# Kernel tuning notes

Hardware: AMD Instinct MI355X
Metric: run time of the kernel (lower is better)

Reference implementation:

```python
import jax, jax.numpy as jnp
import numpy as np

B, S, H, I, L, NH = 1, 256, 384, 1536, 2, 8

def _gelu(x):
    return jax.nn.gelu(x, approximate=False)  # torch nn.GELU default = exact erf

def _ln(x, g, b, eps=1e-5):
    m = x.mean(-1, keepdims=True)
    v = jnp.var(x, axis=-1, keepdims=True)
    return (x - m) / jnp.sqrt(v + eps) * g + b

def _mha(x, Wqkv, bqkv, Wo, bo):
    b_, s_, h_ = x.shape
    d = h_ // NH
    qkv = x @ Wqkv.T + bqkv  # [B,S,3H]
    q, k, v = jnp.split(qkv, 3, axis=-1)
    sp = lambda t: t.reshape(b_, s_, NH, d).transpose(0, 2, 1, 3)  # [B,NH,S,d]
    q, k, v = sp(q), sp(k), sp(v)
    att = jax.nn.softmax(jnp.einsum('bhqd,bhkd->bhqk', q * (1.0 / np.sqrt(d)), k), axis=-1)
    o = jnp.einsum('bhqk,bhkd->bhqd', att, v).transpose(0, 2, 1, 3).reshape(b_, s_, h_)
    return o @ Wo.T + bo

def _forward(hidden_states, Wqkv, bqkv, Wo, bo, W1, b1, W2, b2, g1, be1, g2, be2,
             Wbil, bbil, Wc1, bc1, Wc2, bc2, Wih, bih, Whh, bhh, Wp1, bp1, Wp2, bp2,
             Wout, bout, reasoning_steps):
    x = hidden_states
    rstate = jnp.zeros((x.shape[0], x.shape[-1]), x.dtype)
    cprobs, conts = [], []
    for _ in range(reasoning_steps):
        # symbolic reasoning layers (eval mode: dropout off)
        for l in range(L):
            x = _ln(x + _mha(x, Wqkv[l], bqkv[l], Wo[l], bo[l]), g1[l], be1[l])
            ff = _gelu(x @ W1[l].T + b1[l]) @ W2[l].T + b2[l]
            x = _ln(x + ff, g2[l], be2[l])
        # contradiction detector: bilinear over all token pairs
        tmp = jnp.einsum('bix,oxy->bioy', x, Wbil)            # [B,S,H,H]
        inter = jnp.einsum('bioy,bjy->bijo', tmp, x) + bbil   # [B,S,S,H]
        h1 = _gelu(inter @ Wc1.T + bc1)                       # [B,S,S,H]
        logits = jnp.einsum('bijh,h->bij', h1, Wc2[0]) + bc2[0]
        cprobs.append(jax.nn.sigmoid(logits))
        # recursive reasoning controller (GRUCell on mean-pooled states)
        pooled = x.mean(axis=1)
        gi = pooled @ Wih.T + bih
        gh = rstate @ Whh.T + bhh
        ir, iz, inn = jnp.split(gi, 3, axis=-1)
        hr, hz, hn = jnp.split(gh, 3, axis=-1)
        r = jax.nn.sigmoid(ir + hr)
        z = jax.nn.sigmoid(iz + hz)
        n = jnp.tanh(inn + r * hn)
        rstate = (1.0 - z) * n + z * rstate
        conts.append(jax.nn.sigmoid(_gelu(rstate @ Wp1.T + bp1) @ Wp2[0] + bp2[0]))
    final = x @ Wout.T + bout
    return final, jnp.stack(cprobs), jnp.stack(conts)

def setup_inputs():
    key = jax.random.key(0)
    ks = iter(jax.random.split(key, 40))
    rn = lambda shape, s=0.02: jax.random.normal(next(ks), shape, jnp.float32) * s
    return {
        'hidden_states': jax.random.normal(next(ks), (B, S, H), jnp.float32),
        'Wqkv': rn((L, 3 * H, H)), 'bqkv': jnp.zeros((L, 3 * H)),
        'Wo': rn((L, H, H)), 'bo': jnp.zeros((L, H)),
        'W1': rn((L, I, H)), 'b1': jnp.zeros((L, I)),
        'W2': rn((L, H, I)), 'b2': jnp.zeros((L, H)),
        'g1': jnp.ones((L, H)), 'be1': jnp.zeros((L, H)),
        'g2': jnp.ones((L, H)), 'be2': jnp.zeros((L, H)),
        'Wbil': rn((H, H, H)), 'bbil': jnp.zeros((H,)),
        'Wc1': rn((H, H)), 'bc1': jnp.zeros((H,)),
        'Wc2': rn((1, H)), 'bc2': jnp.zeros((1,)),
        'Wih': rn((3 * H, H)), 'bih': jnp.zeros((3 * H,)),
        'Whh': rn((3 * H, H)), 'bhh': jnp.zeros((3 * H,)),
        'Wp1': rn((H, H)), 'bp1': jnp.zeros((H,)),
        'Wp2': rn((1, H)), 'bp2': jnp.zeros((1,)),
        'Wout': rn((H, H)), 'bout': jnp.zeros((H,)),
        'reasoning_steps': 2,
    }

def reference(hidden_states, Wqkv, bqkv, Wo, bo, W1, b1, W2, b2, g1, be1, g2, be2,
              Wbil, bbil, Wc1, bc1, Wc2, bc2, Wih, bih, Whh, bhh, Wp1, bp1, Wp2, bp2,
              Wout, bout, reasoning_steps):
    return _forward(hidden_states, Wqkv, bqkv, Wo, bo, W1, b1, W2, b2, g1, be1, g2, be2,
                    Wbil, bbil, Wc1, bc1, Wc2, bc2, Wih, bih, Whh, bhh, Wp1, bp1, Wp2, bp2,
                    Wout, bout, reasoning_steps)
```

## Files before the change

### kernel.cpp

```cpp
#include <hip/hip_runtime.h>

typedef __attribute__((ext_vector_type(4))) float f32x4;
typedef __attribute__((ext_vector_type(8))) short s16x8;

#define DEVI __device__ __forceinline__

DEVI float b2f(short s) {
  union { float f; unsigned u; } v; v.u = ((unsigned)(unsigned short)s) << 16; return v.f;
}
DEVI short f2b(float f) {
  union { float f; unsigned u; } v; v.f = f;
  unsigned u = v.u;
  u += 0x7FFFu + ((u >> 16) & 1u);
  return (short)(u >> 16);
}
DEVI float gelu_f(float x) {
  float z2 = 1.5957691216f * x * (1.0f + 0.044715f * x * x);
  float e = __expf(z2);
  float th = 1.0f - 2.0f / (e + 1.0f);
  return 0.5f * x * (1.0f + th);
}
DEVI float sigm_f(float x) { return 1.0f / (1.0f + expf(-x)); }

DEVI void gld16(const short* g, const short* l) {
  __builtin_amdgcn_global_load_lds((const __attribute__((address_space(1))) void*)g,
                                   (__attribute__((address_space(3))) void*)l, 16, 0, 0);
}

template<bool BIAS, bool OUT_BF16>
__global__ __launch_bounds__(512)
void gemm256_k(const short* __restrict__ A, const short* __restrict__ B,
               const float* __restrict__ bias, void* __restrict__ Cv,
               int N, int K,
               long long sA, long long sB, long long sC)
{
  __shared__ short As[2][256 * 32];
  __shared__ short Bs[2][128 * 32];
  const int bz = blockIdx.z;
  const int n0 = blockIdx.x * 128;
  const int t = threadIdx.x, lane = t & 63, wave = t >> 6;
  const int wm = wave >> 1, wn = wave & 1;
  const short* Ab = A + bz * sA;
  const short* Bb = B + bz * sB;
  const int lr = lane >> 2;
  const int lc = (lane & 3) * 8;
  const int fr = lane & 15, fs = lane >> 4;

  f32x4 acc[4][4];
#pragma unroll
  for (int i = 0; i < 4; ++i)
#pragma unroll
    for (int j = 0; j < 4; ++j) acc[i][j] = f32x4{0.f, 0.f, 0.f, 0.f};

  auto stage = [&](int b, int k0) {
#pragma unroll
    for (int q = 0; q < 2; ++q)
      gld16(Ab + (long long)(q * 128 + wave * 16 + lr) * K + k0 + lc,
            &As[b][(q * 128 + wave * 16) * 32]);
    gld16(Bb + (long long)(n0 + wave * 16 + lr) * K + k0 + lc,
          &Bs[b][wave * 16 * 32]);
  };

  const int NT = K >> 5;
  stage(0, 0);
  __syncthreads();
  for (int tt = 0; tt < NT; ++tt) {
    const int cur = tt & 1;
    if (tt + 1 < NT) stage(cur ^ 1, (tt + 1) << 5);
    s16x8 af[4], bfv[4];
#pragma unroll
    for (int i = 0; i < 4; ++i) af[i]  = *(const s16x8*)&As[cur][(wm * 64 + i * 16 + fr) * 32 + fs * 8];
#pragma unroll
    for (int j = 0; j < 4; ++j) bfv[j] = *(const s16x8*)&Bs[cur][(wn * 64 + j * 16 + fr) * 32 + fs * 8];
#pragma unroll
    for (int i = 0; i < 4; ++i)
#pragma unroll
      for (int j = 0; j < 4; ++j)
        acc[i][j] = __builtin_amdgcn_mfma_f32_16x16x32_bf16(af[i], bfv[j], acc[i][j], 0, 0, 0);
    if (tt + 1 < NT) __syncthreads();
  }

#pragma unroll
  for (int i = 0; i < 4; ++i) {
    int rowb = wm * 64 + i * 16 + fs * 4;
#pragma unroll
    for (int j = 0; j < 4; ++j) {
      int col = n0 + wn * 64 + j * 16 + fr;
      float bb = BIAS ? bias[col] : 0.0f;
#pragma unroll
      for (int u = 0; u < 4; ++u) {
        float v = acc[i][j][u] + bb;
        long long off = bz * sC + (long long)(rowb + u) * N + col;
        if constexpr (OUT_BF16) ((short*)Cv)[off] = f2b(v);
        else                    ((float*)Cv)[off] = v;
      }
    }
  }
}

__global__ __launch_bounds__(512)
void h1log256_k(const short* __restrict__ inter, const short* __restrict__ Wc1b,
                const float* __restrict__ bc1, const float* __restrict__ Wc2,
                const float* __restrict__ bc2, float* __restrict__ outp)
{
  __shared__ short As[2][256 * 64];
  __shared__ short Bs[2][128 * 64];
  __shared__ float part[256][2];
  const int ib = blockIdx.x;
  const int t = threadIdx.x, lane = t & 63, wave = t >> 6;
  const int wm = wave >> 1, wn = wave & 1;
  const short* Ab = inter + (long long)ib * 98304;
  const int srow = lane >> 3;
  const int scol = ((lane & 7) ^ srow) * 8;
  const int fr = lane & 15, fs = lane >> 4;

  float lp[16];
#pragma unroll
  for (int e = 0; e < 16; ++e) lp[e] = 0.f;

  for (int n0 = 0; n0 < 384; n0 += 128) {
    f32x4 acc[4][4];
#pragma unroll
    for (int i = 0; i < 4; ++i)
#pragma unroll
      for (int j = 0; j < 4; ++j) acc[i][j] = f32x4{0.f, 0.f, 0.f, 0.f};

    auto stage = [&](int b, int k0) {
#pragma unroll
      for (int q = 0; q < 4; ++q) {
        int c = wave * 4 + q;
        gld16(Ab + (long long)(c * 8 + srow) * 384 + k0 + scol, &As[b][c * 512]);
      }
#pragma unroll
      for (int q = 0; q < 2; ++q) {
        int c = wave * 2 + q;
        gld16(Wc1b + (long long)(n0 + c * 8 + srow) * 384 + k0 + scol, &Bs[b][c * 512]);
      }
    };

    stage(0, 0);
    __syncthreads();
    for (int tt = 0; tt < 6; ++tt) {
      const int cur = tt & 1;
      if (tt + 1 < 6) stage(cur ^ 1, (tt + 1) << 6);
      s16x8 af[4][2], bfv[4][2];
#pragma unroll
      for (int i = 0; i < 4; ++i) {
        int row = wm * 64 + i * 16 + fr;
#pragma unroll
        for (int s = 0; s < 2; ++s)
          af[i][s] = *(const s16x8*)&As[cur][row * 64 + (((s * 4 + fs) ^ (fr & 7)) * 8)];
      }
#pragma unroll
      for (int j = 0; j < 4; ++j) {
        int row = wn * 64 + j * 16 + fr;
#pragma unroll
        for (int s = 0; s < 2; ++s)
          bfv[j][s] = *(const s16x8*)&Bs[cur][row * 64 + (((s * 4 + fs) ^ (fr & 7)) * 8)];
      }
#pragma unroll
      for (int s = 0; s < 2; ++s)
#pragma unroll
        for (int i = 0; i < 4; ++i)
#pragma unroll
          for (int j = 0; j < 4; ++j)
            acc[i][j] = __builtin_amdgcn_mfma_f32_16x16x32_bf16(af[i][s], bfv[j][s], acc[i][j], 0, 0, 0);
      __syncthreads();
    }
#pragma unroll
    for (int i = 0; i < 4; ++i)
#pragma unroll
      for (int j = 0; j < 4; ++j) {
        int col = n0 + wn * 64 + j * 16 + fr;
        float w2 = Wc2[col], b1v = bc1[col];
#pragma unroll
        for (int u = 0; u < 4; ++u)
          lp[i * 4 + u] += gelu_f(acc[i][j][u] + b1v) * w2;
      }
  }
#pragma unroll
  for (int m = 1; m < 16; m <<= 1)
#pragma unroll
    for (int e = 0; e < 16; ++e) lp[e] += __shfl_xor(lp[e], m);
  if (fr == 0) {
#pragma unroll
    for (int e = 0; e < 16; ++e)
      part[wm * 64 + (e >> 2) * 16 + fs * 4 + (e & 3)][wn] = lp[e];
  }
  __syncthreads();
  if (t < 256) outp[ib * 256 + t] = sigm_f(part[t][0] + part[t][1] + bc2[0]);
}

template<bool BIAS, bool GELU_ACT, bool OUT_BF16>
__global__ __launch_bounds__(256)
void gemm64_k(const short* __restrict__ A, const short* __restrict__ B,
              const float* __restrict__ bias, void* __restrict__ Cv,
              int M, int N, int K)
{
  __shared__ short As[2][64 * 64];
  __shared__ short Bs[2][64 * 64];
  const int n0 = blockIdx.x * 64;
  const int m0 = blockIdx.y * 64;
  const int t = threadIdx.x, lane = t & 63, wave = t >> 6;
  const int wm = wave >> 1, wn = wave & 1;
  const int srow = lane >> 3;
  const int scol = ((lane & 7) ^ srow) * 8;
  const int fr = lane & 15, fs = lane >> 4;

  f32x4 acc[2][2];
#pragma unroll
  for (int i = 0; i < 2; ++i)
#pragma unroll
    for (int j = 0; j < 2; ++j) acc[i][j] = f32x4{0.f, 0.f, 0.f, 0.f};

  auto stage = [&](int b, int k0) {
#pragma unroll
    for (int q = 0; q < 2; ++q) {
      int c = wave * 2 + q;
      gld16(A + (long long)(m0 + c * 8 + srow) * K + k0 + scol, &As[b][c * 512]);
      gld16(B + (long long)(n0 + c * 8 + srow) * K + k0 + scol, &Bs[b][c * 512]);
    }
  };

  const int NT = K >> 6;
  stage(0, 0);
  __syncthreads();
  for (int tt = 0; tt < NT; ++tt) {
    const int cur = tt & 1;
    if (tt + 1 < NT) stage(cur ^ 1, (tt + 1) << 6);
    s16x8 af[2][2], bfv[2][2];
#pragma unroll
    for (int i = 0; i < 2; ++i) {
      int row = wm * 32 + i * 16 + fr;
#pragma unroll
      for (int s = 0; s < 2; ++s)
        af[i][s] = *(const s16x8*)&As[cur][row * 64 + (((s * 4 + fs) ^ (fr & 7)) * 8)];
    }
#pragma unroll
    for (int j = 0; j < 2; ++j) {
      int row = wn * 32 + j * 16 + fr;
#pragma unroll
      for (int s = 0; s < 2; ++s)
        bfv[j][s] = *(const s16x8*)&Bs[cur][row * 64 + (((s * 4 + fs) ^ (fr & 7)) * 8)];
    }
#pragma unroll
    for (int s = 0; s < 2; ++s)
#pragma unroll
      for (int i = 0; i < 2; ++i)
#pragma unroll
        for (int j = 0; j < 2; ++j)
          acc[i][j] = __builtin_amdgcn_mfma_f32_16x16x32_bf16(af[i][s], bfv[j][s], acc[i][j], 0, 0, 0);
    if (tt + 1 < NT) __syncthreads();
  }

#pragma unroll
  for (int i = 0; i < 2; ++i) {
    int rowb = m0 + wm * 32 + i * 16 + fs * 4;
#pragma unroll
    for (int j = 0; j < 2; ++j) {
      int col = n0 + wn * 32 + j * 16 + fr;
      float bb = BIAS ? bias[col] : 0.0f;
#pragma unroll
      for (int u = 0; u < 4; ++u) {
        float v = acc[i][j][u] + bb;
        if constexpr (GELU_ACT) v = gelu_f(v);
        long long off = (long long)(rowb + u) * N + col;
        if constexpr (OUT_BF16) ((short*)Cv)[off] = f2b(v);
        else                    ((float*)Cv)[off] = v;
      }
    }
  }
}

__global__ __launch_bounds__(256)
void transpose_k(const float* __restrict__ W, short* __restrict__ WT)
{
  __shared__ short L[64 * 68];
  const int o  = blockIdx.z;
  const int x0 = blockIdx.x * 64, y0 = blockIdx.y * 64;
  const float* Wo = W  + (long long)o * 147456;
  short*      WTo = WT + (long long)o * 147456;
  const int t  = threadIdx.x;
  const int rr = t >> 4;
  const int cc = (t & 15) * 4;
#pragma unroll
  for (int q = 0; q < 4; ++q) {
    int xl = rr + 16 * q;
    float4 v = *(const float4*)(Wo + (x0 + xl) * 384 + y0 + cc);
    short4 p; p.x = f2b(v.x); p.y = f2b(v.y); p.z = f2b(v.z); p.w = f2b(v.w);
    *(short4*)&L[xl * 68 + cc] = p;
  }
  __syncthreads();
#pragma unroll
  for (int q = 0; q < 4; ++q) {
    int yl = rr + 16 * q;
    short4 p;
    p.x = L[(cc + 0) * 68 + yl];
    p.y = L[(cc + 1) * 68 + yl];
    p.z = L[(cc + 2) * 68 + yl];
    p.w = L[(cc + 3) * 68 + yl];
    *(short4*)(WTo + (y0 + yl) * 384 + x0 + cc) = p;
  }
}

__global__ __launch_bounds__(256)
void convall_k(const float* __restrict__ Wc1, const float* __restrict__ Wqkv,
               const float* __restrict__ Wo, const float* __restrict__ W1,
               const float* __restrict__ W2, const float* __restrict__ Wout,
               short* __restrict__ Dc1, short* __restrict__ Dqkv,
               short* __restrict__ Do, short* __restrict__ D1,
               short* __restrict__ D2, short* __restrict__ Dout)
{
  long long i4 = ((long long)blockIdx.x * 256 + threadIdx.x) * 4;
  const float* s; short* d; long long off;
  if      (i4 <  147456) { s = Wc1;  d = Dc1;  off = 0; }
  else if (i4 < 1032192) { s = Wqkv; d = Dqkv; off = 147456; }
  else if (i4 < 1327104) { s = Wo;   d = Do;   off = 1032192; }
  else if (i4 < 2506752) { s = W1;   d = D1;   off = 1327104; }
  else if (i4 < 3686400) { s = W2;   d = D2;   off = 2506752; }
  else if (i4 < 3833856) { s = Wout; d = Dout; off = 3686400; }
  else return;
  long long l = i4 - off;
  float4 v = *(const float4*)(s + l);
  short4 p; p.x = f2b(v.x); p.y = f2b(v.y); p.z = f2b(v.z); p.w = f2b(v.w);
  *(short4*)(d + l) = p;
}

__global__ __launch_bounds__(256)
void attn_k(const float* __restrict__ qkv, short* __restrict__ outb)
{
  __shared__ short Ks[256 * 48];
  __shared__ short Vs[256 * 48];
  __shared__ float Ps[32][258];
  const int h  = blockIdx.y;
  const int q0 = blockIdx.x * 32;
  const int t = threadIdx.x, lane = t & 63, wave = t >> 6;
  for (int idx = t; idx < 3072; idx += 256) {
    int j = idx / 12, d4 = (idx - (idx / 12) * 12) * 4;
    const float* base = qkv + j * 1152 + h * 48 + d4;
    float4 kv = *(const float4*)(base + 384);
    float4 vv = *(const float4*)(base + 768);
    short4 pk; pk.x = f2b(kv.x); pk.y = f2b(kv.y); pk.z = f2b(kv.z); pk.w = f2b(kv.w);
    short4 pv; pv.x = f2b(vv.x); pv.y = f2b(vv.y); pv.z = f2b(vv.z); pv.w = f2b(vv.w);
    *(short4*)&Ks[j * 48 + d4] = pk;
    *(short4*)&Vs[j * 48 + d4] = pv;
  }
  __syncthreads();
  const int part = lane & 7;
  const int rl   = wave * 8 + (lane >> 3);
  const int row  = q0 + rl;
  float q[48];
#pragma unroll
  for (int d = 0; d < 48; ++d) q[d] = qkv[row * 1152 + h * 48 + d] * 0.14433756729740644f;
  float mx = -1e30f;
  for (int jj = 0; jj < 32; ++jj) {
    int j = jj * 8 + part;
    float a = 0.f;
#pragma unroll
    for (int dd = 0; dd < 12; ++dd) {
      short4 kk = *(const short4*)&Ks[j * 48 + dd * 4];
      a += q[dd*4+0]*b2f(kk.x) + q[dd*4+1]*b2f(kk.y) + q[dd*4+2]*b2f(kk.z) + q[dd*4+3]*b2f(kk.w);
    }
    Ps[rl][j] = a;
    mx = fmaxf(mx, a);
  }
  mx = fmaxf(mx, __shfl_xor(mx, 1));
  mx = fmaxf(mx, __shfl_xor(mx, 2));
  mx = fmaxf(mx, __shfl_xor(mx, 4));
  float sum = 0.f;
  for (int jj = 0; jj < 32; ++jj) {
    int j = jj * 8 + part;
    float e = expf(Ps[rl][j] - mx);
    Ps[rl][j] = e;
    sum += e;
  }
  sum += __shfl_xor(sum, 1); sum += __shfl_xor(sum, 2); sum += __shfl_xor(sum, 4);
  const float inv = 1.f / sum;
  __syncthreads();
  float o[6] = {0.f, 0.f, 0.f, 0.f, 0.f, 0.f};
  const int vb = part * 6;
  for (int j = 0; j < 256; ++j) {
    float p = Ps[rl][j];
    int base = j * 48 + vb;
#pragma unroll
    for (int dd = 0; dd < 3; ++dd) {
      short2 vv = *(const short2*)&Vs[base + dd * 2];
      o[dd*2]   += p * b2f(vv.x);
      o[dd*2+1] += p * b2f(vv.y);
    }
  }
#pragma unroll
  for (int d = 0; d < 6; ++d) outb[row * 384 + h * 48 + vb + d] = f2b(o[d] * inv);
}

__global__ __launch_bounds__(128)
void ln_k(const float* __restrict__ x, const short* __restrict__ d,
          const float* __restrict__ g, const float* __restrict__ b,
          float* __restrict__ xo, short* __restrict__ xob)
{
  const int row = blockIdx.x, t = threadIdx.x;
  float v[3]; float s = 0.f, ss = 0.f;
#pragma unroll
  for (int i = 0; i < 3; ++i) {
    int c = t + 128 * i;
    float u = x[row * 384 + c] + b2f(d[row * 384 + c]);
    v[i] = u; s += u; ss += u * u;
  }
#pragma unroll
  for (int m = 1; m < 64; m <<= 1) { s += __shfl_xor(s, m); ss += __shfl_xor(ss, m); }
  __shared__ float sh[4];
  if ((t & 63) == 0) { sh[(t >> 6) * 2] = s; sh[(t >> 6) * 2 + 1] = ss; }
  __syncthreads();
  s = sh[0] + sh[2]; ss = sh[1] + sh[3];
  float mean = s * (1.f / 384.f);
  float var  = ss * (1.f / 384.f) - mean * mean;
  float rstd = rsqrtf(var + 1e-5f);
#pragma unroll
  for (int i = 0; i < 3; ++i) {
    int c = t + 128 * i;
    float y = (v[i] - mean) * rstd * g[c] + b[c];
    xo[row * 384 + c]  = y;
    xob[row * 384 + c] = f2b(y);
  }
}

__global__ void init_k(const float* __restrict__ hs, float* __restrict__ x,
                       short* __restrict__ xb, float* __restrict__ rstate)
{
  int i = blockIdx.x * 256 + threadIdx.x;
  if (i < 98304) { float v = hs[i]; x[i] = v; xb[i] = f2b(v); }
  if (i < 384) rstate[i] = 0.f;
}

__global__ __launch_bounds__(384)
void pool1_k(const float* __restrict__ x, float* __restrict__ partial)
{
  const int t = threadIdx.x, p = blockIdx.x;
  float s = 0.f;
  const float* xr = x + p * 32 * 384;
#pragma unroll 4
  for (int i = 0; i < 32; ++i) s += xr[i * 384 + t];
  partial[p * 384 + t] = s;
}

__global__ __launch_bounds__(256)
void gih_k(const float* __restrict__ Wih, const float* __restrict__ bih,
           const float* __restrict__ Whh, const float* __restrict__ bhh,
           const float* __restrict__ partial, const float* __restrict__ rstate,
           float* __restrict__ gi, float* __restrict__ gh)
{
  const int t = threadIdx.x, lane = t & 63, wave = t >> 6;
  const int r = blockIdx.x * 4 + wave;
  float a = 0.f, b = 0.f;
#pragma unroll
  for (int e = 0; e < 6; ++e) {
    int c = lane + 64 * e;
    float pc = 0.f;
#pragma unroll
    for (int p = 0; p < 8; ++p) pc += partial[p * 384 + c];
    pc *= (1.f / 256.f);
    a += Wih[r * 384 + c] * pc;
    b += Whh[r * 384 + c] * rstate[c];
  }
#pragma unroll
  for (int m = 1; m < 64; m <<= 1) { a += __shfl_xor(a, m); b += __shfl_xor(b, m); }
  if (lane == 0) { gi[r] = a + bih[r]; gh[r] = b + bhh[r]; }
}

__global__ __launch_bounds__(384)
void gru2_k(const float* __restrict__ gi, const float* __restrict__ gh,
            float* __restrict__ rstate, float* __restrict__ hnew)
{
  const int t = threadIdx.x;
  float r = sigm_f(gi[t] + gh[t]);
  float z = sigm_f(gi[384 + t] + gh[384 + t]);
  float n = tanhf(gi[768 + t] + r * gh[768 + t]);
  float h = (1.f - z) * n + z * rstate[t];
  rstate[t] = h;
  hnew[t] = h;
}

__global__ __launch_bounds__(256)
void p1_k(const float* __restrict__ Wp1, const float* __restrict__ bp1,
          const float* __restrict__ hnew, float* __restrict__ p1)
{
  const int t = threadIdx.x, lane = t & 63, wave = t >> 6;
  const int r = blockIdx.x * 4 + wave;
  float a = 0.f;
#pragma unroll
  for (int e = 0; e < 6; ++e) { int c = lane + 64 * e; a += Wp1[r * 384 + c] * hnew[c]; }
#pragma unroll
  for (int m = 1; m < 64; m <<= 1) a += __shfl_xor(a, m);
  if (lane == 0) p1[r] = gelu_f(a + bp1[r]);
}

__global__ __launch_bounds__(64)
void cont_k(const float* __restrict__ p1, const float* __restrict__ Wp2,
            const float* __restrict__ bp2, float* __restrict__ out_cont)
{
  const int lane = threadIdx.x;
  float a = 0.f;
#pragma unroll
  for (int e = 0; e < 6; ++e) { int c = lane + 64 * e; a += p1[c] * Wp2[c]; }
#pragma unroll
  for (int m = 1; m < 64; m <<= 1) a += __shfl_xor(a, m);
  if (lane == 0) out_cont[0] = sigm_f(a + bp2[0]);
}

extern "C" void kernel_launch(void* const* d_in, const int* in_sizes, int n_in,
                              void* d_out, int out_size, void* d_ws, size_t ws_size,
                              hipStream_t stream)
{
  const float* hs   = (const float*)d_in[0];
  const float* Wqkv = (const float*)d_in[1];
  const float* bqkv = (const float*)d_in[2];
  const float* Wo   = (const float*)d_in[3];
  const float* bo   = (const float*)d_in[4];
  const float* W1   = (const float*)d_in[5];
  const float* b1   = (const float*)d_in[6];
  const float* W2   = (const float*)d_in[7];
  const float* b2   = (const float*)d_in[8];
  const float* g1   = (const float*)d_in[9];
  const float* be1  = (const float*)d_in[10];
  const float* g2   = (const float*)d_in[11];
  const float* be2  = (const float*)d_in[12];
  const float* Wbil = (const float*)d_in[13];
  const float* bbil = (const float*)d_in[14];
  const float* Wc1  = (const float*)d_in[15];
  const float* bc1  = (const float*)d_in[16];
  const float* Wc2  = (const float*)d_in[17];
  const float* bc2  = (const float*)d_in[18];
  const float* Wih  = (const float*)d_in[19];
  const float* bih  = (const float*)d_in[20];
  const float* Whh  = (const float*)d_in[21];
  const float* bhh  = (const float*)d_in[22];
  const float* Wp1  = (const float*)d_in[23];
  const float* bp1  = (const float*)d_in[24];
  const float* Wp2  = (const float*)d_in[25];
  const float* bp2  = (const float*)d_in[26];
  const float* Wout = (const float*)d_in[27];
  const float* bout = (const float*)d_in[28];
  float* out = (float*)d_out;

  char* ws = (char*)d_ws;
  size_t off = 0;
  auto alloc = [&](size_t bytes) -> char* {
    char* p = ws + off; off += (bytes + 255) & ~(size_t)255; return p;
  };
  short* wbilT   = (short*)alloc(56623104ULL * 2);
  short* tmp     = (short*)alloc(256ULL * 147456 * 2);
  short* inter   = (short*)alloc(256ULL * 98304 * 2);
  float* x       = (float*)alloc(98304 * 4);
  short* xb      = (short*)alloc(98304 * 2);
  float* qkv     = (float*)alloc(294912 * 4);
  short* attnb   = (short*)alloc(98304 * 2);
  short* deltab  = (short*)alloc(98304 * 2);
  short* ff1b    = (short*)alloc(393216 * 2);
  float* rstate  = (float*)alloc(384 * 4);
  float* partial = (float*)alloc(8 * 384 * 4);
  float* gi      = (float*)alloc(1152 * 4);
  float* gh      = (float*)alloc(1152 * 4);
  float* hnew    = (float*)alloc(384 * 4);
  float* p1buf   = (float*)alloc(384 * 4);
  short* wc1b    = (short*)alloc(147456 * 2);
  short* wqkvb   = (short*)alloc(884736ULL * 2);
  short* wob     = (short*)alloc(294912ULL * 2);
  short* w1b     = (short*)alloc(1179648ULL * 2);
  short* w2b     = (short*)alloc(1179648ULL * 2);
  short* woutb   = (short*)alloc(147456 * 2);
  (void)ws_size; (void)in_sizes; (void)n_in; (void)out_size;

  dim3 B256(256);
  dim3 B512(512);

  init_k<<<dim3(384), B256, 0, stream>>>(hs, x, xb, rstate);
  transpose_k<<<dim3(6, 6, 384), B256, 0, stream>>>(Wbil, wbilT);
  convall_k<<<dim3(3744), B256, 0, stream>>>(Wc1, Wqkv, Wo, W1, W2, Wout,
                                             wc1b, wqkvb, wob, w1b, w2b, woutb);

  for (int s = 0; s < 2; ++s) {
    for (int l = 0; l < 2; ++l) {
      gemm64_k<true, false, false><<<dim3(18, 4), B256, 0, stream>>>(
          xb, wqkvb + l * 442368, bqkv + l * 1152, qkv, 256, 1152, 384);
      attn_k<<<dim3(8, 8), B256, 0, stream>>>(qkv, attnb);
      gemm64_k<true, false, true><<<dim3(6, 4), B256, 0, stream>>>(
          attnb, wob + l * 147456, bo + l * 384, deltab, 256, 384, 384);
      ln_k<<<dim3(256), dim3(128), 0, stream>>>(x, deltab, g1 + l * 384, be1 + l * 384, x, xb);
      gemm64_k<true, true, true><<<dim3(24, 4), B256, 0, stream>>>(
          xb, w1b + l * 589824, b1 + l * 1536, ff1b, 256, 1536, 384);
      gemm64_k<true, false, true><<<dim3(6, 4), B256, 0, stream>>>(
          ff1b, w2b + l * 589824, b2 + l * 384, deltab, 256, 384, 1536);
      ln_k<<<dim3(256), dim3(128), 0, stream>>>(x, deltab, g2 + l * 384, be2 + l * 384, x, xb);
    }
    gemm256_k<false, true><<<dim3(1152, 1, 1), B512, 0, stream>>>(
        xb, wbilT, (const float*)nullptr, tmp, 147456, 384, 0, 0, 0);
    gemm256_k<true, true><<<dim3(3, 1, 256), B512, 0, stream>>>(
        xb, tmp, bbil, inter, 384, 384, 0, 147456LL, 98304LL);
    h1log256_k<<<dim3(256), B512, 0, stream>>>(inter, wc1b, bc1, Wc2, bc2,
                                               out + 98304 + s * 65536);
    pool1_k<<<dim3(8), dim3(384), 0, stream>>>(x, partial);
    gih_k<<<dim3(288), B256, 0, stream>>>(Wih, bih, Whh, bhh, partial, rstate, gi, gh);
    gru2_k<<<dim3(1), dim3(384), 0, stream>>>(gi, gh, rstate, hnew);
    p1_k<<<dim3(96), B256, 0, stream>>>(Wp1, bp1, hnew, p1buf);
    cont_k<<<dim3(1), dim3(64), 0, stream>>>(p1buf, Wp2, bp2, out + 98304 + 131072 + s);
  }
  gemm64_k<true, false, false><<<dim3(6, 4), B256, 0, stream>>>(
      xb, woutb, bout, out, 256, 384, 384);
}
```

Baseline: 607.4 us.

## Fold GRU controller kernels into bilinear GEMM and h1 logit launches

The mean-pool partial sums are now computed by 8 extra blocks appended to the first bilinear GEMM. The GRU input and hidden projections run as 144 extra blocks appended to the h1/logit kernel. The GRU cell update is merged into the Wp1 projection kernel, which needs ping-pong rstate buffers so blocks can read the old state while writing the new one. This removes three small serial launches per reasoning step and lets the tiny controller work overlap with the big GEMMs. In exchange, the extra branches add divergent block roles inside heavy kernels, and every p1m block recomputes the GRU gates redundantly.

```diff
diff --git a/kernel.cpp b/kernel.cpp
--- a/kernel.cpp
+++ b/kernel.cpp
@@ -25,6 +25,86 @@
 DEVI void gld16(const short* g, const short* l) {
   __builtin_amdgcn_global_load_lds((const __attribute__((address_space(1))) void*)g,
                                    (__attribute__((address_space(3))) void*)l, 16, 0, 0);
+}
+
+template<bool BIAS, bool OUT_BF16>
+__global__ __launch_bounds__(512)
+void gemm256pool_k(const short* __restrict__ A, const short* __restrict__ B,
+                   const float* __restrict__ bias, void* __restrict__ Cv,
+                   int N, int K, int nblk,
+                   const float* __restrict__ xfull, float* __restrict__ partial)
+{
+  const int t = threadIdx.x;
+  if ((int)blockIdx.x >= nblk) {
+    const int p = blockIdx.x - nblk;
+    if (t < 384) {
+      float s = 0.f;
+      const float* xr = xfull + p * 32 * 384;
+#pragma unroll 4
+      for (int i = 0; i < 32; ++i) s += xr[i * 384 + t];
+      partial[p * 384 + t] = s;
+    }
+    return;
+  }
+  __shared__ short As[2][256 * 32];
+  __shared__ short Bs[2][128 * 32];
+  const int n0 = blockIdx.x * 128;
+  const int lane = t & 63, wave = t >> 6;
+  const int wm = wave >> 1, wn = wave & 1;
+  const int lr = lane >> 2;
+  const int lc = (lane & 3) * 8;
+  const int fr = lane & 15, fs = lane >> 4;
+
+  f32x4 acc[4][4];
+#pragma unroll
+  for (int i = 0; i < 4; ++i)
+#pragma unroll
+    for (int j = 0; j < 4; ++j) acc[i][j] = f32x4{0.f, 0.f, 0.f, 0.f};
+
+  auto stage = [&](int b, int k0) {
+#pragma unroll
+    for (int q = 0; q < 2; ++q)
+      gld16(A + (long long)(q * 128 + wave * 16 + lr) * K + k0 + lc,
+            &As[b][(q * 128 + wave * 16) * 32]);
+    gld16(B + (long long)(n0 + wave * 16 + lr) * K + k0 + lc,
+          &Bs[b][wave * 16 * 32]);
+  };
+
+  const int NT = K >> 5;
+  stage(0, 0);
+  __syncthreads();
+  for (int tt = 0; tt < NT; ++tt) {
+    const int cur = tt & 1;
+    if (tt + 1 < NT) stage(cur ^ 1, (tt + 1) << 5);
+    s16x8 af[4], bfv[4];
+#pragma unroll
+    for (int i = 0; i < 4; ++i) af[i]  = *(const s16x8*)&As[cur][(wm * 64 + i * 16 + fr) * 32 + fs * 8];
+#pragma unroll
+    for (int j = 0; j < 4; ++j) bfv[j] = *(const s16x8*)&Bs[cur][(wn * 64 + j * 16 + fr) * 32 + fs * 8];
+#pragma unroll
+    for (int i = 0; i < 4; ++i)
+#pragma unroll
+      for (int j = 0; j < 4; ++j)
+        acc[i][j] = __builtin_amdgcn_mfma_f32_16x16x32_bf16(af[i], bfv[j], acc[i][j], 0, 0, 0);
+    if (tt + 1 < NT) __syncthreads();
+  }
+
+#pragma unroll
+  for (int i = 0; i < 4; ++i) {
+    int rowb = wm * 64 + i * 16 + fs * 4;
+#pragma unroll
+    for (int j = 0; j < 4; ++j) {
+      int col = n0 + wn * 64 + j * 16 + fr;
+      float bb = BIAS ? bias[col] : 0.0f;
+#pragma unroll
+      for (int u = 0; u < 4; ++u) {
+        float v = acc[i][j][u] + bb;
+        long long off = (long long)(rowb + u) * N + col;
+        if constexpr (OUT_BF16) ((short*)Cv)[off] = f2b(v);
+        else                    ((float*)Cv)[off] = v;
+      }
+    }
+  }
 }
 
 template<bool BIAS, bool OUT_BF16>
@@ -101,13 +181,35 @@
 __global__ __launch_bounds__(512)
 void h1log256_k(const short* __restrict__ inter, const short* __restrict__ Wc1b,
                 const float* __restrict__ bc1, const float* __restrict__ Wc2,
-                const float* __restrict__ bc2, float* __restrict__ outp)
-{
+                const float* __restrict__ bc2, float* __restrict__ outp,
+                const float* __restrict__ Wih, const float* __restrict__ bih,
+                const float* __restrict__ Whh, const float* __restrict__ bhh,
+                const float* __restrict__ partial, const float* __restrict__ rs0,
+                float* __restrict__ gi, float* __restrict__ gh)
+{
+  const int t = threadIdx.x, lane = t & 63, wave = t >> 6;
+  if ((int)blockIdx.x >= 256) {
+    const int r = (blockIdx.x - 256) * 8 + wave;
+    float a = 0.f, b = 0.f;
+#pragma unroll
+    for (int e = 0; e < 6; ++e) {
+      int c = lane + 64 * e;
+      float pc = 0.f;
+#pragma unroll
+      for (int p = 0; p < 8; ++p) pc += partial[p * 384 + c];
+      pc *= (1.f / 256.f);
+      a += Wih[r * 384 + c] * pc;
+      b += Whh[r * 384 + c] * rs0[c];
+    }
+#pragma unroll
+    for (int m = 1; m < 64; m <<= 1) { a += __shfl_xor(a, m); b += __shfl_xor(b, m); }
+    if (lane == 0) { gi[r] = a + bih[r]; gh[r] = b + bhh[r]; }
+    return;
+  }
   __shared__ short As[2][256 * 64];
   __shared__ short Bs[2][128 * 64];
   __shared__ float part[256][2];
   const int ib = blockIdx.x;
-  const int t = threadIdx.x, lane = t & 63, wave = t >> 6;
   const int wm = wave >> 1, wn = wave & 1;
   const short* Ab = inter + (long long)ib * 98304;
   const int srow = lane >> 3;
@@ -429,69 +531,33 @@
 {
   int i = blockIdx.x * 256 + threadIdx.x;
   if (i < 98304) { float v = hs[i]; x[i] = v; xb[i] = f2b(v); }
-  if (i < 384) rstate[i] = 0.f;
-}
-
-__global__ __launch_bounds__(384)
-void pool1_k(const float* __restrict__ x, float* __restrict__ partial)
-{
-  const int t = threadIdx.x, p = blockIdx.x;
-  float s = 0.f;
-  const float* xr = x + p * 32 * 384;
-#pragma unroll 4
-  for (int i = 0; i < 32; ++i) s += xr[i * 384 + t];
-  partial[p * 384 + t] = s;
+  if (i < 768) rstate[i] = 0.f;
 }
 
 __global__ __launch_bounds__(256)
-void gih_k(const float* __restrict__ Wih, const float* __restrict__ bih,
-           const float* __restrict__ Whh, const float* __restrict__ bhh,
-           const float* __restrict__ partial, const float* __restrict__ rstate,
-           float* __restrict__ gi, float* __restrict__ gh)
-{
+void p1m_k(const float* __restrict__ gi, const float* __restrict__ gh,
+           const float* __restrict__ rs0, float* __restrict__ rs1,
+           const float* __restrict__ Wp1, const float* __restrict__ bp1,
+           float* __restrict__ p1)
+{
+  __shared__ float hn[384];
   const int t = threadIdx.x, lane = t & 63, wave = t >> 6;
-  const int r = blockIdx.x * 4 + wave;
-  float a = 0.f, b = 0.f;
-#pragma unroll
-  for (int e = 0; e < 6; ++e) {
-    int c = lane + 64 * e;
-    float pc = 0.f;
-#pragma unroll
-    for (int p = 0; p < 8; ++p) pc += partial[p * 384 + c];
-    pc *= (1.f / 256.f);
-    a += Wih[r * 384 + c] * pc;
-    b += Whh[r * 384 + c] * rstate[c];
-  }
-#pragma unroll
-  for (int m = 1; m < 64; m <<= 1) { a += __shfl_xor(a, m); b += __shfl_xor(b, m); }
-  if (lane == 0) { gi[r] = a + bih[r]; gh[r] = b + bhh[r]; }
-}
-
-__global__ __launch_bounds__(384)
-void gru2_k(const float* __restrict__ gi, const float* __restrict__ gh,
-            float* __restrict__ rstate, float* __restrict__ hnew)
-{
-  const int t = threadIdx.x;
-  float r = sigm_f(gi[t] + gh[t]);
-  float z = sigm_f(gi[384 + t] + gh[384 + t]);
-  float n = tanhf(gi[768 + t] + r * gh[768 + t]);
-  float h = (1.f - z) * n + z * rstate[t];
-  rstate[t] = h;
-  hnew[t] = h;
-}
-
-__global__ __launch_bounds__(256)
-void p1_k(const float* __restrict__ Wp1, const float* __restrict__ bp1,
-          const float* __restrict__ hnew, float* __restrict__ p1)
-{
-  const int t = threadIdx.x, lane = t & 63, wave = t >> 6;
+  for (int c = t; c < 384; c += 256) {
+    float r = sigm_f(gi[c] + gh[c]);
+    float z = sigm_f(gi[384 + c] + gh[384 + c]);
+    float n = tanhf(gi[768 + c] + r * gh[768 + c]);
+    hn[c] = (1.f - z) * n + z * rs0[c];
+  }
+  __syncthreads();
   const int r = blockIdx.x * 4 + wave;
   float a = 0.f;
 #pragma unroll
-  for (int e = 0; e < 6; ++e) { int c = lane + 64 * e; a += Wp1[r * 384 + c] * hnew[c]; }
+  for (int e = 0; e < 6; ++e) { int c = lane + 64 * e; a += Wp1[r * 384 + c] * hn[c]; }
 #pragma unroll
   for (int m = 1; m < 64; m <<= 1) a += __shfl_xor(a, m);
   if (lane == 0) p1[r] = gelu_f(a + bp1[r]);
+  if (blockIdx.x == 0)
+    for (int c = t; c < 384; c += 256) rs1[c] = hn[c];
 }
 
 __global__ __launch_bounds__(64)
@@ -556,11 +622,10 @@
   short* attnb   = (short*)alloc(98304 * 2);
   short* deltab  = (short*)alloc(98304 * 2);
   short* ff1b    = (short*)alloc(393216 * 2);
-  float* rstate  = (float*)alloc(384 * 4);
+  float* rstate  = (float*)alloc(768 * 4);
   float* partial = (float*)alloc(8 * 384 * 4);
   float* gi      = (float*)alloc(1152 * 4);
   float* gh      = (float*)alloc(1152 * 4);
-  float* hnew    = (float*)alloc(384 * 4);
   float* p1buf   = (float*)alloc(384 * 4);
   short* wc1b    = (short*)alloc(147456 * 2);
   short* wqkvb   = (short*)alloc(884736ULL * 2);
@@ -579,6 +644,8 @@
                                              wc1b, wqkvb, wob, w1b, w2b, woutb);
 
   for (int s = 0; s < 2; ++s) {
+    float* rs0 = rstate + (s & 1) * 384;
+    float* rs1 = rstate + ((s + 1) & 1) * 384;
     for (int l = 0; l < 2; ++l) {
       gemm64_k<true, false, false><<<dim3(18, 4), B256, 0, stream>>>(
           xb, wqkvb + l * 442368, bqkv + l * 1152, qkv, 256, 1152, 384);
@@ -592,16 +659,14 @@
           ff1b, w2b + l * 589824, b2 + l * 384, deltab, 256, 384, 1536);
       ln_k<<<dim3(256), dim3(128), 0, stream>>>(x, deltab, g2 + l * 384, be2 + l * 384, x, xb);
     }
-    gemm256_k<false, true><<<dim3(1152, 1, 1), B512, 0, stream>>>(
-        xb, wbilT, (const float*)nullptr, tmp, 147456, 384, 0, 0, 0);
+    gemm256pool_k<false, true><<<dim3(1160), B512, 0, stream>>>(
+        xb, wbilT, (const float*)nullptr, tmp, 147456, 384, 1152, x, partial);
     gemm256_k<true, true><<<dim3(3, 1, 256), B512, 0, stream>>>(
         xb, tmp, bbil, inter, 384, 384, 0, 147456LL, 98304LL);
-    h1log256_k<<<dim3(256), B512, 0, stream>>>(inter, wc1b, bc1, Wc2, bc2,
-                                               out + 98304 + s * 65536);
-    pool1_k<<<dim3(8), dim3(384), 0, stream>>>(x, partial);
-    gih_k<<<dim3(288), B256, 0, stream>>>(Wih, bih, Whh, bhh, partial, rstate, gi, gh);
-    gru2_k<<<dim3(1), dim3(384), 0, stream>>>(gi, gh, rstate, hnew);
-    p1_k<<<dim3(96), B256, 0, stream>>>(Wp1, bp1, hnew, p1buf);
+    h1log256_k<<<dim3(400), B512, 0, stream>>>(inter, wc1b, bc1, Wc2, bc2,
+                                               out + 98304 + s * 65536,
+                                               Wih, bih, Whh, bhh, partial, rs0, gi, gh);
+    p1m_k<<<dim3(96), B256, 0, stream>>>(gi, gh, rs0, rs1, Wp1, bp1, p1buf);
     cont_k<<<dim3(1), dim3(64), 0, stream>>>(p1buf, Wp2, bp2, out + 98304 + 131072 + s);
   }
   gemm64_k<true, false, false><<<dim3(6, 4), B256, 0, stream>>>(
```

New measurement: 593.7 us. 2.3% less time.
